# Performance work log

Hardware: AMD Instinct MI355X
Metric: run time of the kernel (lower is better)

## Reference

```python
import jax, jax.numpy as jnp
import numpy as np
import math

N = 50000   # nodes
E = 800000  # edges
D = 128     # in_channels == out_channels
SLOPE = 0.1
BN_EPS = 1e-5


def setup_inputs() -> dict:
    key = jax.random.key(0)
    k1, k2, k3 = jax.random.split(key, 3)
    x = jax.random.normal(k1, (N, D), jnp.float32)
    edge_index = jax.random.randint(k2, (2, E), 0, N, jnp.int32)
    # xavier_uniform with leaky_relu gain, as in reset_parameters
    gain = math.sqrt(2.0 / (1.0 + SLOPE ** 2))
    bound = gain * math.sqrt(6.0 / (D + D))
    W = jax.random.uniform(k3, (D, D), jnp.float32, -bound, bound)  # lin.weight [out,in]
    bias = jnp.zeros((D,), jnp.float32)
    gamma = jnp.ones((D,), jnp.float32)
    beta = jnp.zeros((D,), jnp.float32)
    return {"x": x, "W": W, "bias": bias, "gamma": gamma, "beta": beta,
            "edge_index": edge_index}


def reference(x, W, bias, gamma, beta, edge_index):
    n = x.shape[0]
    residual = x  # shortcut is Identity (in_channels == out_channels)

    loops = jnp.arange(n, dtype=edge_index.dtype)
    self_loops = jnp.stack([loops, loops])

    # forward() manually adds self-loops and computes symmetric norm (edge_weight)
    ei1 = jnp.concatenate([edge_index, self_loops], axis=1)
    row1, col1 = ei1[0], ei1[1]
    deg = jax.ops.segment_sum(jnp.ones_like(row1, x.dtype), row1, n)
    dis = jnp.where(deg > 0, jax.lax.rsqrt(jnp.where(deg > 0, deg, 1.0)), 0.0)
    w1 = dis[row1] * dis[col1]

    # GCNConv(normalize=True, improved=True) internally re-runs gcn_norm:
    # adds another set of self-loops with fill_value 2.0, recomputes sym norm
    ei2 = jnp.concatenate([ei1, self_loops], axis=1)
    w2 = jnp.concatenate([w1, jnp.full((n,), 2.0, x.dtype)])
    row2, col2 = ei2[0], ei2[1]
    deg2 = jax.ops.segment_sum(w2, col2, n)
    dis2 = jnp.where(deg2 > 0, jax.lax.rsqrt(jnp.where(deg2 > 0, deg2, 1.0)), 0.0)
    norm = dis2[row2] * w2 * dis2[col2]

    # linear transform then gather-scale-scatter aggregation
    h = x @ W.T                                           # [N, D]
    agg = jax.ops.segment_sum(norm[:, None] * h[row2], col2, n) + bias

    # BatchNorm1d (training-mode batch stats), LeakyReLU, dropout (eval=identity)
    mu = agg.mean(axis=0)
    var = agg.var(axis=0)
    bn = (agg - mu) * jax.lax.rsqrt(var + BN_EPS) * gamma + beta
    act = jax.nn.leaky_relu(bn, SLOPE)
    return jax.nn.leaky_relu(act + residual, SLOPE)
```

## Files before the change

### kernel.cpp

```cpp
#include <hip/hip_runtime.h>
#include <hip/hip_fp16.h>

constexpr float SLOPE = 0.1f;
constexpr float BN_EPS = 1e-5f;
constexpr int BCAP = 8192;
constexpr int CHUNK = 4096;
constexpr int BKT = 1024;
constexpr int EPT = CHUNK / BKT;

typedef __attribute__((ext_vector_type(8))) short bf16x8;
typedef __attribute__((ext_vector_type(4))) float f32x4;
typedef __attribute__((ext_vector_type(2))) float f32x2;

__device__ inline unsigned bf16rn(float f) {
    unsigned b = __float_as_uint(f);
    return (b + 0x7fffu + ((b >> 16) & 1u)) >> 16;
}

__device__ inline unsigned h2u(__half2 h) { return *(unsigned*)&h; }
__device__ inline __half2 u2h(unsigned u) { return *(__half2*)&u; }

__global__ void k_zero(int* __restrict__ p, int n) {
    int i = blockIdx.x * blockDim.x + threadIdx.x;
    if (i < n) p[i] = 0;
}

__global__ __launch_bounds__(1024) void k_bucket3(const int* __restrict__ row,
                                                  const int* __restrict__ col, int E,
                                                  int* __restrict__ bcnt, int* __restrict__ rcnt,
                                                  unsigned* __restrict__ bdat,
                                                  unsigned char* __restrict__ rdat, int NB) {
    __shared__ unsigned sdata[CHUNK];
    __shared__ int cnt[256];
    __shared__ int off[256];
    __shared__ int gbase[256];
    __shared__ int wsum[4];
    int t = threadIdx.x;
    int l = t & 63, w = t >> 6;
    int base = blockIdx.x * CHUNK;
    int r[EPT], c[EPT];
#pragma unroll
    for (int k = 0; k < EPT; ++k) {
        int i = base + k * BKT + t;
        if (i < E) { r[k] = row[i]; c[k] = col[i]; } else { r[k] = -1; c[k] = 0; }
    }
    if (t < 256) cnt[t] = 0;
    __syncthreads();
#pragma unroll
    for (int k = 0; k < EPT; ++k) if (r[k] >= 0) atomicAdd(&cnt[c[k] >> 8], 1);
    __syncthreads();
    int v = (t < 256) ? cnt[t] : 0, inc = v;
#pragma unroll
    for (int d = 1; d < 64; d <<= 1) { int u = __shfl_up(inc, d); if (l >= d) inc += u; }
    if (t < 256 && l == 63) wsum[w] = inc;
    __syncthreads();
    if (t < 256) {
        int p = 0;
        for (int i = 0; i < w; ++i) p += wsum[i];
        off[t] = p + inc - v;
        cnt[t] = 0;
    }
    __syncthreads();
#pragma unroll
    for (int k = 0; k < EPT; ++k) if (r[k] >= 0) {
        int bb = c[k] >> 8;
        int pos = off[bb] + atomicAdd(&cnt[bb], 1);
        sdata[pos] = ((unsigned)r[k] << 8) | (unsigned)(c[k] & 255);
    }
    __syncthreads();
    if (t < NB) gbase[t] = atomicAdd(&bcnt[t * 16], cnt[t]);
    __syncthreads();
    for (int b = w; b < NB; b += 16) {
        int cb = cnt[b];
        if (cb == 0) continue;
        int gb = gbase[b];
        int lim = min(cb, BCAP - gb);
        unsigned* dst = bdat + (size_t)b * BCAP + gb;
        const unsigned* src = &sdata[off[b]];
        for (int i = l; i < lim; i += 64) dst[i] = src[i];
    }
    __syncthreads();
    unsigned char* sb = (unsigned char*)sdata;
    if (t < 256) cnt[t] = 0;
    __syncthreads();
#pragma unroll
    for (int k = 0; k < EPT; ++k) if (r[k] >= 0) atomicAdd(&cnt[r[k] >> 8], 1);
    __syncthreads();
    v = (t < 256) ? cnt[t] : 0; inc = v;
#pragma unroll
    for (int d = 1; d < 64; d <<= 1) { int u = __shfl_up(inc, d); if (l >= d) inc += u; }
    if (t < 256 && l == 63) wsum[w] = inc;
    __syncthreads();
    if (t < 256) {
        int p = 0;
        for (int i = 0; i < w; ++i) p += wsum[i];
        off[t] = p + inc - v;
        cnt[t] = 0;
    }
    __syncthreads();
#pragma unroll
    for (int k = 0; k < EPT; ++k) if (r[k] >= 0) {
        int rb = r[k] >> 8;
        int pos = off[rb] + atomicAdd(&cnt[rb], 1);
        sb[pos] = (unsigned char)(r[k] & 255);
    }
    __syncthreads();
    if (t < NB) gbase[t] = atomicAdd(&rcnt[t * 16], cnt[t]);
    __syncthreads();
    for (int b = w; b < NB; b += 16) {
        int cb = cnt[b];
        if (cb == 0) continue;
        int gb = gbase[b];
        int lim = min(cb, BCAP - gb);
        unsigned char* dst = rdat + (size_t)b * BCAP + gb;
        const unsigned char* src = &sb[off[b]];
        for (int i = l; i < lim; i += 64) dst[i] = src[i];
    }
}

__global__ __launch_bounds__(512) void k_outdeg(const int* __restrict__ rcnt,
                                                const unsigned char* __restrict__ rdat,
                                                float* __restrict__ dis, int N) {
    __shared__ int hist[256];
    int b = blockIdx.x, t = threadIdx.x;
    if (t < 256) hist[t] = 0;
    __syncthreads();
    int cnt = min(rcnt[b * 16], BCAP);
    const unsigned char* p = rdat + (size_t)b * BCAP;
    const unsigned* p4 = (const unsigned*)p;
    int nw = cnt >> 2;
    for (int i = t; i < nw; i += 512) {
        unsigned v = p4[i];
        atomicAdd(&hist[v & 255u], 1);
        atomicAdd(&hist[(v >> 8) & 255u], 1);
        atomicAdd(&hist[(v >> 16) & 255u], 1);
        atomicAdd(&hist[v >> 24], 1);
    }
    for (int i = nw * 4 + t; i < cnt; i += 512) atomicAdd(&hist[p[i]], 1);
    __syncthreads();
    if (t < 256) {
        int node = b * 256 + t;
        if (node < N) dis[node] = rsqrtf((float)(hist[t] + 1));
    }
}

__global__ __launch_bounds__(512) void k_deg2(const int* __restrict__ bcnt,
                                              const unsigned* __restrict__ bdat,
                                              const float* __restrict__ dis,
                                              int* __restrict__ csr_off,
                                              float* __restrict__ dw,
                                              float* __restrict__ selfw, int N, int NB) {
    __shared__ int   hist[256];
    __shared__ float fsum[256];
    __shared__ int   sm2[256];
    __shared__ int   sm2x[256];
    __shared__ int   wsum[4];
    int b = blockIdx.x, t = threadIdx.x;
    int l = t & 63, w = t >> 6;
    if (t < 256) {
        sm2[t] = (t < NB) ? min(bcnt[t * 16], BCAP) : 0;
        hist[t] = 0;
        fsum[t] = 0.0f;
    }
    __syncthreads();
    int v = (t < 256) ? sm2[t] : 0, inc = v;
#pragma unroll
    for (int d = 1; d < 64; d <<= 1) { int u = __shfl_up(inc, d); if (l >= d) inc += u; }
    if (t < 256 && l == 63) wsum[w] = inc;
    __syncthreads();
    if (t < 256) {
        int p = 0;
        for (int i = 0; i < w; ++i) p += wsum[i];
        sm2x[t] = p + inc - v;
    }
    __syncthreads();
    if (b == 0 && t == 0) csr_off[N] = sm2x[NB - 1] + sm2[NB - 1];
    int bb = sm2x[b];
    int cnt = min(bcnt[b * 16], BCAP);
    const unsigned* p = bdat + (size_t)b * BCAP;
    for (int i = t; i < cnt; i += 512) {
        unsigned e = p[i];
        int c = (int)(e & 255u);
        atomicAdd(&hist[c], 1);
        atomicAdd(&fsum[c], dis[e >> 8]);
    }
    __syncthreads();
    v = (t < 256) ? hist[t] : 0; inc = v;
#pragma unroll
    for (int d = 1; d < 64; d <<= 1) { int u = __shfl_up(inc, d); if (l >= d) inc += u; }
    if (t < 256 && l == 63) wsum[w] = inc;
    __syncthreads();
    if (t < 256) {
        int p2 = 0;
        for (int i = 0; i < w; ++i) p2 += wsum[i];
        int node = b * 256 + t;
        if (node < N) {
            csr_off[node] = bb + p2 + inc - v;
            float ds = dis[node];
            float deg2 = 2.0f + ds * ds + ds * fsum[t];
            dw[node] = ds * rsqrtf(deg2);
            selfw[node] = (ds * ds + 2.0f) / deg2;
        }
    }
}

__global__ __launch_bounds__(512) void k_csr2(const int* __restrict__ bcnt,
                                              const unsigned* __restrict__ bdat,
                                              const int* __restrict__ csr_off,
                                              const float* __restrict__ dw,
                                              unsigned* __restrict__ csr, int N, int NB) {
    __shared__ int   tick[256];
    __shared__ int   base[256];
    __shared__ float dwl[256];
    int b = blockIdx.x, t = threadIdx.x;
    if (t < 256) {
        tick[t] = 0;
        int node = b * 256 + t;
        base[t] = (node < N) ? csr_off[node] : 0;
        dwl[t]  = (node < N) ? dw[node] : 0.0f;
    }
    __syncthreads();
    int cnt = min(bcnt[b * 16], BCAP);
    const unsigned* p = bdat + (size_t)b * BCAP;
    for (int i = t; i < cnt; i += 512) {
        unsigned e = p[i];
        int c = (int)(e & 255u);
        int r = (int)(e >> 8);
        float wgt = dw[r] * dwl[c];
        int pos = base[c] + atomicAdd(&tick[c], 1);
        unsigned hb = (unsigned)__half_as_ushort(__float2half_rn(wgt));
        csr[pos] = ((unsigned)r << 16) | hb;
    }
}

__global__ __launch_bounds__(256) void k_gemm(const float* __restrict__ x,
                                              const float* __restrict__ W,
                                              unsigned* __restrict__ h16,
                                              unsigned* __restrict__ h8, int N) {
    __shared__ unsigned short wb[128 * 136];
    int tx = threadIdx.x;
    for (int idx = tx; idx < 128 * 64; idx += 256) {
        int d = idx >> 6;
        int kp = (idx & 63) * 2;
        float2 wv = *(const float2*)&W[d * 128 + kp];
        wb[d * 136 + kp]     = (unsigned short)bf16rn(wv.x);
        wb[d * 136 + kp + 1] = (unsigned short)bf16rn(wv.y);
    }
    __syncthreads();
    int wave = tx >> 6, l = tx & 63;
    int lr = l & 15, kg = l >> 4;
    int row = blockIdx.x * 64 + wave * 16 + lr;
    int rclamp = min(row, N - 1);
    f32x4 acc[8];
#pragma unroll
    for (int ct = 0; ct < 8; ++ct) acc[ct] = (f32x4){0.f, 0.f, 0.f, 0.f};
#pragma unroll
    for (int kt = 0; kt < 4; ++kt) {
        int k0 = kt * 32 + kg * 8;
        float xv[8];
        *(float4*)&xv[0] = *(const float4*)&x[(size_t)rclamp * 128 + k0];
        *(float4*)&xv[4] = *(const float4*)&x[(size_t)rclamp * 128 + k0 + 4];
        bf16x8 a;
#pragma unroll
        for (int j = 0; j < 8; ++j) a[j] = (short)bf16rn(xv[j]);
#pragma unroll
        for (int ct = 0; ct < 8; ++ct) {
            bf16x8 bfr = *(const bf16x8*)&wb[(ct * 16 + lr) * 136 + k0];
            acc[ct] = __builtin_amdgcn_mfma_f32_16x16x32_bf16(a, bfr, acc[ct], 0, 0, 0);
        }
    }
    int rowbase = blockIdx.x * 64 + wave * 16 + kg * 4;
#pragma unroll
    for (int ct = 0; ct < 8; ++ct) {
#pragma unroll
        for (int reg = 0; reg < 4; ++reg) {
            float v = acc[ct][reg];
            float p1 = __shfl_xor(v, 1);
            float p2 = __shfl_xor(v, 2);
            float p3 = __shfl_xor(v, 3);
            int orow = rowbase + reg;
            if (orow < N) {
                if ((l & 1) == 0) {
                    unsigned a0 = (unsigned)__half_as_ushort(__float2half_rn(v));
                    unsigned a1 = (unsigned)__half_as_ushort(__float2half_rn(p1));
                    h16[(size_t)orow * 64 + ct * 8 + (lr >> 1)] = a0 | (a1 << 16);
                }
                if ((l & 3) == 0) {
                    int wpk = 0;
                    wpk = __builtin_amdgcn_cvt_pk_fp8_f32(v, p1, wpk, false);
                    wpk = __builtin_amdgcn_cvt_pk_fp8_f32(p2, p3, wpk, true);
                    h8[(size_t)orow * 32 + ct * 4 + (lr >> 2)] = (unsigned)wpk;
                }
            }
        }
    }
}

__global__ __launch_bounds__(256) void k_agg(const uint2* __restrict__ h8,
                                             const uint4* __restrict__ h16,
                                             const int* __restrict__ csr_off,
                                             const unsigned* __restrict__ csr,
                                             const float* __restrict__ selfw,
                                             uint4* __restrict__ agg16, int N) {
    int wv = threadIdx.x >> 6;
    int l = threadIdx.x & 63;
    int ep = l >> 4;
    int sl = l & 15;
    int j = blockIdx.x * 4 + wv;
    if (j >= N) return;
    float acc[8] = {};
    int s0 = csr_off[j], s1 = csr_off[j + 1];
    for (int s = s0 + ep; s < s1; s += 16) {
        int sB = s + 4, sC = s + 8, sD = s + 12;
        unsigned eA = csr[s];
        unsigned eB = (sB < s1) ? csr[sB] : eA;
        unsigned eC = (sC < s1) ? csr[sC] : eA;
        unsigned eD = (sD < s1) ? csr[sD] : eA;
        float wA = __half2float(__ushort_as_half((unsigned short)(eA & 0xffffu)));
        float wB = (sB < s1) ? __half2float(__ushort_as_half((unsigned short)(eB & 0xffffu))) : 0.0f;
        float wC = (sC < s1) ? __half2float(__ushort_as_half((unsigned short)(eC & 0xffffu))) : 0.0f;
        float wD = (sD < s1) ? __half2float(__ushort_as_half((unsigned short)(eD & 0xffffu))) : 0.0f;
        uint2 aA = h8[(size_t)(eA >> 16) * 16 + sl];
        uint2 aB = h8[(size_t)(eB >> 16) * 16 + sl];
        uint2 aC = h8[(size_t)(eC >> 16) * 16 + sl];
        uint2 aD = h8[(size_t)(eD >> 16) * 16 + sl];
#define PACC(aa, ww) { \
        f32x2 q0 = __builtin_amdgcn_cvt_pk_f32_fp8((int)aa.x, false); \
        f32x2 q1 = __builtin_amdgcn_cvt_pk_f32_fp8((int)aa.x, true);  \
        f32x2 q2 = __builtin_amdgcn_cvt_pk_f32_fp8((int)aa.y, false); \
        f32x2 q3 = __builtin_amdgcn_cvt_pk_f32_fp8((int)aa.y, true);  \
        acc[0] += ww * q0.x; acc[1] += ww * q0.y; \
        acc[2] += ww * q1.x; acc[3] += ww * q1.y; \
        acc[4] += ww * q2.x; acc[5] += ww * q2.y; \
        acc[6] += ww * q3.x; acc[7] += ww * q3.y; }
        PACC(aA, wA)
        PACC(aB, wB)
        PACC(aC, wC)
        PACC(aD, wD)
#undef PACC
    }
#pragma unroll
    for (int k = 0; k < 8; ++k) {
        acc[k] += __shfl_xor(acc[k], 16);
        acc[k] += __shfl_xor(acc[k], 32);
    }
    if (ep == 0) {
        float sw = selfw[j];
        uint4 hv = h16[(size_t)j * 16 + sl];
        const __half2* hp = (const __half2*)&hv;
#pragma unroll
        for (int k = 0; k < 4; ++k) {
            float2 f = __half22float2(hp[k]);
            acc[2 * k]     += sw * f.x;
            acc[2 * k + 1] += sw * f.y;
        }
        uint4 o;
        o.x = h2u(__floats2half2_rn(acc[0], acc[1]));
        o.y = h2u(__floats2half2_rn(acc[2], acc[3]));
        o.z = h2u(__floats2half2_rn(acc[4], acc[5]));
        o.w = h2u(__floats2half2_rn(acc[6], acc[7]));
        agg16[(size_t)j * 16 + sl] = o;
    }
}

__global__ __launch_bounds__(1024) void k_stats(const __half2* __restrict__ agg2,
                                                float* __restrict__ sums, int N) {
    __shared__ float ls[256];
    int t = threadIdx.x;
    if (t < 256) ls[t] = 0.0f;
    __syncthreads();
    int d = t & 63;
    int stream = blockIdx.x * 16 + (t >> 6);
    int nstreams = gridDim.x * 16;
    float s0 = 0.f, s1 = 0.f, q0 = 0.f, q1 = 0.f;
    for (int i = stream; i < N; i += nstreams) {
        float2 f = __half22float2(agg2[(size_t)i * 64 + d]);
        s0 += f.x; s1 += f.y;
        q0 += f.x * f.x; q1 += f.y * f.y;
    }
    atomicAdd(&ls[2 * d], s0);
    atomicAdd(&ls[2 * d + 1], s1);
    atomicAdd(&ls[128 + 2 * d], q0);
    atomicAdd(&ls[128 + 2 * d + 1], q1);
    __syncthreads();
    if (t < 256) atomicAdd(&sums[t], ls[t]);
}

__global__ void k_final(const uint2* __restrict__ agg16, const float* __restrict__ x,
                        const float* __restrict__ sums, const float* __restrict__ gamma,
                        const float* __restrict__ beta, float* __restrict__ out,
                        int total4, int N) {
    __shared__ float sc[128], sh[128];
    int t = threadIdx.x;
    if (t < 128) {
        float invN = 1.0f / (float)N;
        float mu = sums[t] * invN;
        float var = sums[128 + t] * invN - mu * mu;
        float s = gamma[t] * rsqrtf(var + BN_EPS);
        sc[t] = s;
        sh[t] = beta[t] - mu * s;
    }
    __syncthreads();
    int idx = blockIdx.x * blockDim.x + t;
    if (idx >= total4) return;
    int c4 = (idx & 31) * 4;
    uint2 a2 = agg16[idx];
    float2 f0 = __half22float2(u2h(a2.x));
    float2 f1 = __half22float2(u2h(a2.y));
    float4 xv = *(const float4*)&x[(size_t)idx * 4];
    float ap[4] = {f0.x, f0.y, f1.x, f1.y};
    float xp[4] = {xv.x, xv.y, xv.z, xv.w};
    float op[4];
#pragma unroll
    for (int j = 0; j < 4; ++j) {
        int d = c4 + j;
        float bn = ap[j] * sc[d] + sh[d];
        float act = bn > 0.0f ? bn : SLOPE * bn;
        float v = act + xp[j];
        op[j] = v > 0.0f ? v : SLOPE * v;
    }
    *(float4*)&out[(size_t)idx * 4] = make_float4(op[0], op[1], op[2], op[3]);
}

extern "C" void kernel_launch(void* const* d_in, const int* in_sizes, int n_in,
                              void* d_out, int out_size, void* d_ws, size_t ws_size,
                              hipStream_t stream) {
    const float* x     = (const float*)d_in[0];
    const float* W     = (const float*)d_in[1];
    const float* gamma = (const float*)d_in[3];
    const float* beta  = (const float*)d_in[4];
    const int*   ei    = (const int*)d_in[5];
    int N = in_sizes[0] / 128;
    int E = in_sizes[5] / 2;
    const int* row = ei;
    const int* col = ei + E;
    float* out = (float*)d_out;

    int NB = (N + 255) >> 8;

    char* ws = (char*)d_ws;
    size_t off = 0;
    auto alloc = [&](size_t b) { size_t o = off; off = (off + b + 255) & ~(size_t)255; return o; };
    size_t o_sums  = alloc(512 * 4);
    size_t o_bcnt  = alloc((size_t)NB * 16 * 4);
    size_t o_rcnt  = alloc((size_t)NB * 16 * 4);
    size_t zbytes  = off;
    size_t o_bdat  = alloc((size_t)NB * BCAP * 4);
    size_t o_rdat  = alloc((size_t)NB * BCAP);
    size_t o_dis   = alloc((size_t)N * 4);
    size_t o_dw    = alloc((size_t)N * 4);
    size_t o_selfw = alloc((size_t)N * 4);
    size_t o_coff  = alloc((size_t)(N + 1) * 4);
    size_t o_crow  = alloc((size_t)E * 4);
    size_t o_h16   = alloc((size_t)N * 128 * 2);
    size_t o_h8    = alloc((size_t)N * 128);
    size_t o_agg   = alloc((size_t)N * 128 * 2);
    if (ws_size < off) return;

    float*         sums    = (float*)(ws + o_sums);
    int*           bcnt    = (int*)(ws + o_bcnt);
    int*           rcnt    = (int*)(ws + o_rcnt);
    unsigned*      bdat    = (unsigned*)(ws + o_bdat);
    unsigned char* rdat    = (unsigned char*)(ws + o_rdat);
    float*         dis     = (float*)(ws + o_dis);
    float*         dw      = (float*)(ws + o_dw);
    float*         selfw   = (float*)(ws + o_selfw);
    int*           csr_off = (int*)(ws + o_coff);
    unsigned*      csr     = (unsigned*)(ws + o_crow);
    unsigned*      h16     = (unsigned*)(ws + o_h16);
    unsigned*      h8      = (unsigned*)(ws + o_h8);
    unsigned*      agg     = (unsigned*)(ws + o_agg);

    int NBLK = (E + CHUNK - 1) / CHUNK;
    int zn = (int)(zbytes / 4);

    k_zero<<<(zn + 255) / 256, 256, 0, stream>>>((int*)ws, zn);
    k_bucket3<<<NBLK, BKT, 0, stream>>>(row, col, E, bcnt, rcnt, bdat, rdat, NB);
    k_outdeg<<<NB, 512, 0, stream>>>(rcnt, rdat, dis, N);
    k_deg2<<<NB, 512, 0, stream>>>(bcnt, bdat, dis, csr_off, dw, selfw, N, NB);
    k_csr2<<<NB, 512, 0, stream>>>(bcnt, bdat, csr_off, dw, csr, N, NB);
    k_gemm<<<(N + 63) / 64, 256, 0, stream>>>(x, W, h16, h8, N);
    k_agg<<<(N + 3) / 4, 256, 0, stream>>>((const uint2*)h8, (const uint4*)h16, csr_off, csr, selfw, (uint4*)agg, N);
    k_stats<<<128, 1024, 0, stream>>>((const __half2*)agg, sums, N);
    int total4 = N * 32;
    k_final<<<(total4 + 255) / 256, 256, 0, stream>>>((const uint2*)agg, x, sums, gamma, beta, out, total4, N);
}
```

Before: 115.2 us.

## Quantize gathered node features to 4-bit FP4 with per-row scale folded into edge weights

The gathered feature table used in aggregation shrinks from FP8 (128 B/row) to a 4-bit e2m1-style code (64 B/row) with a per-row absmax scale. The scale is folded into the source-side normalization factor, so the CSR edge weights carry it. The CSR build now runs after the GEMM. Aggregation decodes nibble pairs through a shared-memory lookup table, aiming to halve the random-gather traffic. This adds quantization error on neighbor contributions, plus LDS lookups and extra GEMM epilogue work.

Result: slower. 128.9 us (+12.0%).

```diff
diff --git a/kernel.cpp b/kernel.cpp
--- a/kernel.cpp
+++ b/kernel.cpp
@@ -10,7 +10,6 @@
 
 typedef __attribute__((ext_vector_type(8))) short bf16x8;
 typedef __attribute__((ext_vector_type(4))) float f32x4;
-typedef __attribute__((ext_vector_type(2))) float f32x2;
 
 __device__ inline unsigned bf16rn(float f) {
     unsigned b = __float_as_uint(f);
@@ -204,40 +203,14 @@
     }
 }
 
-__global__ __launch_bounds__(512) void k_csr2(const int* __restrict__ bcnt,
-                                              const unsigned* __restrict__ bdat,
-                                              const int* __restrict__ csr_off,
-                                              const float* __restrict__ dw,
-                                              unsigned* __restrict__ csr, int N, int NB) {
-    __shared__ int   tick[256];
-    __shared__ int   base[256];
-    __shared__ float dwl[256];
-    int b = blockIdx.x, t = threadIdx.x;
-    if (t < 256) {
-        tick[t] = 0;
-        int node = b * 256 + t;
-        base[t] = (node < N) ? csr_off[node] : 0;
-        dwl[t]  = (node < N) ? dw[node] : 0.0f;
-    }
-    __syncthreads();
-    int cnt = min(bcnt[b * 16], BCAP);
-    const unsigned* p = bdat + (size_t)b * BCAP;
-    for (int i = t; i < cnt; i += 512) {
-        unsigned e = p[i];
-        int c = (int)(e & 255u);
-        int r = (int)(e >> 8);
-        float wgt = dw[r] * dwl[c];
-        int pos = base[c] + atomicAdd(&tick[c], 1);
-        unsigned hb = (unsigned)__half_as_ushort(__float2half_rn(wgt));
-        csr[pos] = ((unsigned)r << 16) | hb;
-    }
-}
-
 __global__ __launch_bounds__(256) void k_gemm(const float* __restrict__ x,
                                               const float* __restrict__ W,
+                                              const float* __restrict__ dw,
                                               unsigned* __restrict__ h16,
-                                              unsigned* __restrict__ h8, int N) {
+                                              unsigned* __restrict__ h4,
+                                              float* __restrict__ dws, int N) {
     __shared__ unsigned short wb[128 * 136];
+    __shared__ unsigned char ebytes[64][128];
     int tx = threadIdx.x;
     for (int idx = tx; idx < 128 * 64; idx += 256) {
         int d = idx >> 6;
@@ -276,34 +249,97 @@
         for (int reg = 0; reg < 4; ++reg) {
             float v = acc[ct][reg];
             float p1 = __shfl_xor(v, 1);
-            float p2 = __shfl_xor(v, 2);
-            float p3 = __shfl_xor(v, 3);
             int orow = rowbase + reg;
-            if (orow < N) {
-                if ((l & 1) == 0) {
-                    unsigned a0 = (unsigned)__half_as_ushort(__float2half_rn(v));
-                    unsigned a1 = (unsigned)__half_as_ushort(__float2half_rn(p1));
-                    h16[(size_t)orow * 64 + ct * 8 + (lr >> 1)] = a0 | (a1 << 16);
-                }
-                if ((l & 3) == 0) {
-                    int wpk = 0;
-                    wpk = __builtin_amdgcn_cvt_pk_fp8_f32(v, p1, wpk, false);
-                    wpk = __builtin_amdgcn_cvt_pk_fp8_f32(p2, p3, wpk, true);
-                    h8[(size_t)orow * 32 + ct * 4 + (lr >> 2)] = (unsigned)wpk;
-                }
+            if ((l & 1) == 0 && orow < N) {
+                unsigned a0 = (unsigned)__half_as_ushort(__float2half_rn(v));
+                unsigned a1 = (unsigned)__half_as_ushort(__float2half_rn(p1));
+                h16[(size_t)orow * 64 + ct * 8 + (lr >> 1)] = a0 | (a1 << 16);
             }
         }
     }
-}
-
-__global__ __launch_bounds__(256) void k_agg(const uint2* __restrict__ h8,
+#pragma unroll
+    for (int reg = 0; reg < 4; ++reg) {
+        float am = 0.0f;
+#pragma unroll
+        for (int ct = 0; ct < 8; ++ct) am = fmaxf(am, fabsf(acc[ct][reg]));
+#pragma unroll
+        for (int d = 1; d < 16; d <<= 1) am = fmaxf(am, __shfl_xor(am, d));
+        float s = am * (1.0f / 6.0f);
+        float inv = (am > 0.0f) ? 6.0f / am : 0.0f;
+        int orow = rowbase + reg;
+        if (lr == 0 && orow < N) dws[orow] = dw[orow] * s;
+        int rowl = wave * 16 + kg * 4 + reg;
+#pragma unroll
+        for (int ct = 0; ct < 8; ++ct) {
+            float vv = acc[ct][reg];
+            float a = fabsf(vv) * inv;
+            int n = (a > 0.25f) + (a > 0.75f) + (a > 1.25f) + (a > 1.75f)
+                  + (a > 2.5f) + (a > 3.5f) + (a > 5.0f);
+            ebytes[rowl][ct * 16 + lr] = (unsigned char)(((vv < 0.0f) ? 8 : 0) | n);
+        }
+    }
+    __syncthreads();
+    for (int idx = tx; idx < 1024; idx += 256) {
+        int rowl = idx >> 4, dwi = idx & 15;
+        int orow = blockIdx.x * 64 + rowl;
+        if (orow >= N) continue;
+        const unsigned char* eb = &ebytes[rowl][dwi * 8];
+        unsigned pk = 0;
+#pragma unroll
+        for (int k = 0; k < 4; ++k)
+            pk |= ((unsigned)(eb[2 * k] | (eb[2 * k + 1] << 4))) << (8 * k);
+        h4[(size_t)orow * 16 + dwi] = pk;
+    }
+}
+
+__global__ __launch_bounds__(512) void k_csr2(const int* __restrict__ bcnt,
+                                              const unsigned* __restrict__ bdat,
+                                              const int* __restrict__ csr_off,
+                                              const float* __restrict__ dws,
+                                              const float* __restrict__ dw,
+                                              unsigned* __restrict__ csr, int N, int NB) {
+    __shared__ int   tick[256];
+    __shared__ int   base[256];
+    __shared__ float dwl[256];
+    int b = blockIdx.x, t = threadIdx.x;
+    if (t < 256) {
+        tick[t] = 0;
+        int node = b * 256 + t;
+        base[t] = (node < N) ? csr_off[node] : 0;
+        dwl[t]  = (node < N) ? dw[node] : 0.0f;
+    }
+    __syncthreads();
+    int cnt = min(bcnt[b * 16], BCAP);
+    const unsigned* p = bdat + (size_t)b * BCAP;
+    for (int i = t; i < cnt; i += 512) {
+        unsigned e = p[i];
+        int c = (int)(e & 255u);
+        int r = (int)(e >> 8);
+        float wgt = dws[r] * dwl[c];
+        int pos = base[c] + atomicAdd(&tick[c], 1);
+        unsigned hb = (unsigned)__half_as_ushort(__float2half_rn(wgt));
+        csr[pos] = ((unsigned)r << 16) | hb;
+    }
+}
+
+__global__ __launch_bounds__(256) void k_agg(const unsigned* __restrict__ h4,
                                              const uint4* __restrict__ h16,
                                              const int* __restrict__ csr_off,
                                              const unsigned* __restrict__ csr,
                                              const float* __restrict__ selfw,
                                              uint4* __restrict__ agg16, int N) {
-    int wv = threadIdx.x >> 6;
-    int l = threadIdx.x & 63;
+    __shared__ float2 lut[256];
+    int t = threadIdx.x;
+    if (t < 256) {
+        const float g[8] = {0.f, 0.5f, 1.f, 1.5f, 2.f, 3.f, 4.f, 6.f};
+        int lo = t & 15, hi = t >> 4;
+        float vlo = g[lo & 7] * ((lo & 8) ? -1.f : 1.f);
+        float vhi = g[hi & 7] * ((hi & 8) ? -1.f : 1.f);
+        lut[t] = make_float2(vlo, vhi);
+    }
+    __syncthreads();
+    int wv = t >> 6;
+    int l = t & 63;
     int ep = l >> 4;
     int sl = l & 15;
     int j = blockIdx.x * 4 + wv;
@@ -320,15 +356,15 @@
         float wB = (sB < s1) ? __half2float(__ushort_as_half((unsigned short)(eB & 0xffffu))) : 0.0f;
         float wC = (sC < s1) ? __half2float(__ushort_as_half((unsigned short)(eC & 0xffffu))) : 0.0f;
         float wD = (sD < s1) ? __half2float(__ushort_as_half((unsigned short)(eD & 0xffffu))) : 0.0f;
-        uint2 aA = h8[(size_t)(eA >> 16) * 16 + sl];
-        uint2 aB = h8[(size_t)(eB >> 16) * 16 + sl];
-        uint2 aC = h8[(size_t)(eC >> 16) * 16 + sl];
-        uint2 aD = h8[(size_t)(eD >> 16) * 16 + sl];
+        unsigned aA = h4[(size_t)(eA >> 16) * 16 + sl];
+        unsigned aB = h4[(size_t)(eB >> 16) * 16 + sl];
+        unsigned aC = h4[(size_t)(eC >> 16) * 16 + sl];
+        unsigned aD = h4[(size_t)(eD >> 16) * 16 + sl];
 #define PACC(aa, ww) { \
-        f32x2 q0 = __builtin_amdgcn_cvt_pk_f32_fp8((int)aa.x, false); \
-        f32x2 q1 = __builtin_amdgcn_cvt_pk_f32_fp8((int)aa.x, true);  \
-        f32x2 q2 = __builtin_amdgcn_cvt_pk_f32_fp8((int)aa.y, false); \
-        f32x2 q3 = __builtin_amdgcn_cvt_pk_f32_fp8((int)aa.y, true);  \
+        float2 q0 = lut[aa & 255u]; \
+        float2 q1 = lut[(aa >> 8) & 255u]; \
+        float2 q2 = lut[(aa >> 16) & 255u]; \
+        float2 q3 = lut[aa >> 24]; \
         acc[0] += ww * q0.x; acc[1] += ww * q0.y; \
         acc[2] += ww * q1.x; acc[3] += ww * q1.y; \
         acc[4] += ww * q2.x; acc[5] += ww * q2.y; \
@@ -449,11 +485,12 @@
     size_t o_rdat  = alloc((size_t)NB * BCAP);
     size_t o_dis   = alloc((size_t)N * 4);
     size_t o_dw    = alloc((size_t)N * 4);
+    size_t o_dws   = alloc((size_t)N * 4);
     size_t o_selfw = alloc((size_t)N * 4);
     size_t o_coff  = alloc((size_t)(N + 1) * 4);
     size_t o_crow  = alloc((size_t)E * 4);
     size_t o_h16   = alloc((size_t)N * 128 * 2);
-    size_t o_h8    = alloc((size_t)N * 128);
+    size_t o_h4    = alloc((size_t)N * 64);
     size_t o_agg   = alloc((size_t)N * 128 * 2);
     if (ws_size < off) return;
 
@@ -464,11 +501,12 @@
     unsigned char* rdat    = (unsigned char*)(ws + o_rdat);
     float*         dis     = (float*)(ws + o_dis);
     float*         dw      = (float*)(ws + o_dw);
+    float*         dws     = (float*)(ws + o_dws);
     float*         selfw   = (float*)(ws + o_selfw);
     int*           csr_off = (int*)(ws + o_coff);
     unsigned*      csr     = (unsigned*)(ws + o_crow);
     unsigned*      h16     = (unsigned*)(ws + o_h16);
-    unsigned*      h8      = (unsigned*)(ws + o_h8);
+    unsigned*      h4      = (unsigned*)(ws + o_h4);
     unsigned*      agg     = (unsigned*)(ws + o_agg);
 
     int NBLK = (E + CHUNK - 1) / CHUNK;
@@ -478,9 +516,9 @@
     k_bucket3<<<NBLK, BKT, 0, stream>>>(row, col, E, bcnt, rcnt, bdat, rdat, NB);
     k_outdeg<<<NB, 512, 0, stream>>>(rcnt, rdat, dis, N);
     k_deg2<<<NB, 512, 0, stream>>>(bcnt, bdat, dis, csr_off, dw, selfw, N, NB);
-    k_csr2<<<NB, 512, 0, stream>>>(bcnt, bdat, csr_off, dw, csr, N, NB);
-    k_gemm<<<(N + 63) / 64, 256, 0, stream>>>(x, W, h16, h8, N);
-    k_agg<<<(N + 3) / 4, 256, 0, stream>>>((const uint2*)h8, (const uint4*)h16, csr_off, csr, selfw, (uint4*)agg, N);
+    k_gemm<<<(N + 63) / 64, 256, 0, stream>>>(x, W, dw, h16, h4, dws, N);
+    k_csr2<<<NB, 512, 0, stream>>>(bcnt, bdat, csr_off, dws, dw, csr, N, NB);
+    k_agg<<<(N + 3) / 4, 256, 0, stream>>>(h4, (const uint4*)h16, csr_off, csr, selfw, (uint4*)agg, N);
     k_stats<<<128, 1024, 0, stream>>>((const __half2*)agg, sums, N);
     int total4 = N * 32;
     k_final<<<(total4 + 255) / 256, 256, 0, stream>>>((const uint2*)agg, x, sums, gamma, beta, out, total4, N);
```
